# Kernel optimization log

Measured on AMD Instinct MI355X. Metric: run time of the kernel, lower is better.

The kernel has to match this reference:

```python
import jax, jax.numpy as jnp
import numpy as np

DIM = 1024
HEADS = 16
HEAD_DIM = DIM // HEADS
HIDDEN = 4096  # mlp_ratio * dim
SCALE = HEAD_DIM ** -0.5
LN_EPS = 1e-5


def softmax_one(x):
    # softmax with +1 in the denominator (after max subtraction), per source
    m = jnp.max(x, axis=-1, keepdims=True)
    e = jnp.exp(x - m)
    return e / (1.0 + jnp.sum(e, axis=-1, keepdims=True))


def layer_norm(x, g, b):
    mu = jnp.mean(x, axis=-1, keepdims=True)
    var = jnp.mean(jnp.square(x - mu), axis=-1, keepdims=True)
    return (x - mu) * jax.lax.rsqrt(var + LN_EPS) * g + b


def setup_inputs() -> dict:
    key = jax.random.key(0)
    ks = jax.random.split(key, 12)
    B, C, N = 2, DIM, 2048
    x = jax.random.normal(ks[0], (B, C, N), dtype=jnp.float32)
    mask = jax.random.randint(ks[1], (B, HEADS, N), 0, 2, dtype=jnp.int32)
    s = 0.02
    return {
        'x': x,
        'mask': mask,
        'qkv_w': jax.random.normal(ks[2], (3 * DIM, DIM), jnp.float32) * s,
        'qkv_b': jnp.zeros((3 * DIM,), jnp.float32),
        'proj_w': jax.random.normal(ks[3], (DIM, DIM), jnp.float32) * s,
        'proj_b': jnp.zeros((DIM,), jnp.float32),
        'fc1_w': jax.random.normal(ks[4], (HIDDEN, DIM), jnp.float32) * s,
        'fc1_b': jnp.zeros((HIDDEN,), jnp.float32),
        'ln_g': jnp.ones((HIDDEN,), jnp.float32),
        'ln_b': jnp.zeros((HIDDEN,), jnp.float32),
        'fc2_w': jax.random.normal(ks[5], (DIM, HIDDEN), jnp.float32) * s,
        'fc2_b': jnp.zeros((DIM,), jnp.float32),
    }


def reference(x, mask, qkv_w, qkv_b, proj_w, proj_b, fc1_w, fc1_b, ln_g, ln_b, fc2_w, fc2_b):
    B, C, N = x.shape
    xt = jnp.swapaxes(x, 1, 2)  # (B, N, C)

    # ----- attention -----
    qkv = xt @ qkv_w.T + qkv_b                      # (B, N, 3C)
    qkv = qkv.reshape(B, N, 3, HEADS, HEAD_DIM)
    qkv = jnp.transpose(qkv, (2, 0, 3, 1, 4))       # (3, B, H, N, Dh)
    q, k, v = qkv[0], qkv[1], qkv[2]
    scores = jnp.einsum('bhnd,bhmd->bhnm', q * SCALE, k)  # (B, H, N, N)
    scores = jnp.where(mask[:, :, :, None] == 0, -1e9, scores)
    attn = softmax_one(scores)
    out = jnp.einsum('bhnm,bhmd->bhnd', attn, v)    # (B, H, N, Dh)
    # faithful to source: permute(0,3,1,2).reshape(B,N,C) -> scrambled merge
    out = jnp.transpose(out, (0, 3, 1, 2)).reshape(B, N, C)
    out = out @ proj_w.T + proj_b

    # faithful residual: attn_out + ls1(attn_out) with ls1 = Identity
    h = out + out                                   # (B, N, C)

    # ----- MLP (timm Mlp: fc1 -> GELU -> LayerNorm -> fc2) -----
    m = h @ fc1_w.T + fc1_b
    m = jax.nn.gelu(m, approximate=False)
    m = layer_norm(m, ln_g, ln_b)
    m = m @ fc2_w.T + fc2_b
    y = h + m                                       # (B, N, C)

    return jnp.swapaxes(y, 1, 2)                    # (B, C, N)
```

## Files before the change

kernel.cpp:

```cpp
#include <hip/hip_runtime.h>
#include <math.h>

#define DIMC   1024
#define NTOK   2048
#define BATCH  2
#define HEADS  16
#define HDIM   64
#define HIDDEN 4096
#define MROWS  (BATCH*NTOK)
#define QSZ    ((size_t)BATCH*HEADS*NTOK*HDIM)
#define QSC    0.18033688f

typedef unsigned short ushort_t;
typedef __attribute__((ext_vector_type(8))) short short8;
typedef __attribute__((ext_vector_type(4))) float f32x4;
typedef __attribute__((ext_vector_type(4))) unsigned short us4;

__device__ __forceinline__ ushort_t f2b(float f) {
  union { float f; unsigned int u; } cv; cv.f = f;
  unsigned int u = cv.u;
  unsigned int r = (u + 0x7fffu + ((u >> 16) & 1u)) >> 16;
  return (ushort_t)r;
}

__device__ __forceinline__ float b2f(ushort_t b) {
  union { unsigned int u; float f; } cv; cv.u = ((unsigned int)b) << 16;
  return cv.f;
}

__device__ __forceinline__ float fexp2(float x) {
#if __has_builtin(__builtin_amdgcn_exp2f)
  return __builtin_amdgcn_exp2f(x);
#else
  return exp2f(x);
#endif
}

__device__ __forceinline__ void gl_lds16(const void* g, void* l) {
  __builtin_amdgcn_global_load_lds(
      (const __attribute__((address_space(1))) void*)g,
      (__attribute__((address_space(3))) void*)l, 16, 0, 0);
}

__global__ __launch_bounds__(256) void k_transpose(const float* __restrict__ x,
                                                   ushort_t* __restrict__ xt) {
  __shared__ float t[32][33];
  int b  = blockIdx.z;
  int c0 = blockIdx.y * 32, n0 = blockIdx.x * 32;
  int tx = threadIdx.x, ty = threadIdx.y;
#pragma unroll
  for (int l = 0; l < 4; l++)
    t[ty + l * 8][tx] = x[((size_t)(b * DIMC + c0 + ty + l * 8)) * NTOK + n0 + tx];
  __syncthreads();
#pragma unroll
  for (int l = 0; l < 4; l++)
    xt[((size_t)(b * NTOK + n0 + ty + l * 8)) * DIMC + c0 + tx] = f2b(t[tx][ty + l * 8]);
}

__global__ __launch_bounds__(256) void k_f2b4(const float* __restrict__ w0,
                                              const float* __restrict__ w1,
                                              const float* __restrict__ w2,
                                              const float* __restrict__ w3,
                                              ushort_t* __restrict__ o0,
                                              ushort_t* __restrict__ o1,
                                              ushort_t* __restrict__ o2,
                                              ushort_t* __restrict__ o3) {
  int bid = blockIdx.x;
  const float* in; ushort_t* out; int base;
  if (bid < 3072)      { in = w0; out = o0; base = bid; }
  else if (bid < 4096) { in = w1; out = o1; base = bid - 3072; }
  else if (bid < 8192) { in = w2; out = o2; base = bid - 4096; }
  else                 { in = w3; out = o3; base = bid - 8192; }
  int i = base * 256 + threadIdx.x;
  float4 v = ((const float4*)in)[i];
  us4 o; o.x = f2b(v.x); o.y = f2b(v.y); o.z = f2b(v.z); o.w = f2b(v.w);
  ((us4*)out)[i] = o;
}

template <int EPI, int NTX8, int KSTRIDE, int KLEN>
__global__ __launch_bounds__(256) void k_gemm_bf16(const ushort_t* __restrict__ A,
                                                   const ushort_t* __restrict__ W,
                                                   const float* __restrict__ bias,
                                                   void* __restrict__ outv) {
  __shared__ ushort_t As[2][128 * 32];
  __shared__ ushort_t Bs[2][128 * 32];
  const int tid = threadIdx.x;
  const int lane = tid & 63, wv = tid >> 6;
  const int bid = blockIdx.x, kz = blockIdx.y;
  const int xcd = bid & 7, t = bid >> 3;
  const int row0 = (t / NTX8) * 128;
  const int col0 = (xcd * NTX8 + (t % NTX8)) * 128;
  const int wrow0 = (wv >> 1) * 64, wcol0 = (wv & 1) * 64;
  const int lm = lane & 15, lq = lane >> 4;
  const int srow = wv * 32 + (lane >> 2);
  const int gch = (lane & 3) ^ ((lane >> 3) & 3);
  const int sw8 = (lq ^ ((lm >> 1) & 3)) * 8;

  const ushort_t* Ab = A + (size_t)(row0 + srow) * KSTRIDE + (size_t)kz * KLEN + gch * 8;
  const ushort_t* Wb = W + (size_t)(col0 + srow) * KSTRIDE + (size_t)kz * KLEN + gch * 8;
  const size_t rstep = (size_t)16 * KSTRIDE;

  f32x4 acc[4][4];
#pragma unroll
  for (int i = 0; i < 4; i++)
#pragma unroll
    for (int j = 0; j < 4; j++) acc[i][j] = (f32x4){0.f, 0.f, 0.f, 0.f};

#define STAGE(buf, k0) do {                                      \
    gl_lds16(Ab + (k0),         &As[buf][wv * 1024]);            \
    gl_lds16(Ab + rstep + (k0), &As[buf][wv * 1024 + 512]);      \
    gl_lds16(Wb + (k0),         &Bs[buf][wv * 1024]);            \
    gl_lds16(Wb + rstep + (k0), &Bs[buf][wv * 1024 + 512]);      \
  } while (0)

  auto compute = [&](int buf) {
    short8 af[4], bf[4];
#pragma unroll
    for (int mi = 0; mi < 4; mi++)
      af[mi] = *(const short8*)&As[buf][(wrow0 + mi * 16 + lm) * 32 + sw8];
#pragma unroll
    for (int ni = 0; ni < 4; ni++)
      bf[ni] = *(const short8*)&Bs[buf][(wcol0 + ni * 16 + lm) * 32 + sw8];
#pragma unroll
    for (int mi = 0; mi < 4; mi++)
#pragma unroll
      for (int ni = 0; ni < 4; ni++)
        acc[mi][ni] = __builtin_amdgcn_mfma_f32_16x16x32_bf16(af[mi], bf[ni], acc[mi][ni], 0, 0, 0);
  };

  constexpr int S = KLEN / 32;
  STAGE(0, 0);
#pragma unroll 1
  for (int kk = 0; kk < S; kk++) {
    __syncthreads();
    if (kk + 1 < S) STAGE((kk + 1) & 1, (kk + 1) * 32);
    compute(kk & 1);
  }
#undef STAGE

#pragma unroll
  for (int mi = 0; mi < 4; mi++) {
#pragma unroll
    for (int ni = 0; ni < 4; ni++) {
#pragma unroll
      for (int r = 0; r < 4; r++) {
        const int row = row0 + wrow0 + mi * 16 + lq * 4 + r;
        const int col = col0 + wcol0 + ni * 16 + lm;
        float v = acc[mi][ni][r];
        if (EPI != 4) v += bias[col];
        if (EPI == 0) {
          int which = col >> 10, rem = col & 1023, hh = rem >> 6, d = rem & 63;
          int bb = row >> 11, n = row & 2047;
          size_t bh = (size_t)(bb * HEADS + hh);
          ushort_t* o16 = (ushort_t*)outv;
          if (which == 0)
            o16[(bh * NTOK + n) * HDIM + d] = f2b(v * QSC);
          else if (which == 1)
            o16[QSZ + (bh * NTOK + n) * HDIM + d] = f2b(v);
          else
            o16[2 * QSZ + (bh * HDIM + d) * NTOK + n] = f2b(v);
        } else if (EPI == 2) {
          ((ushort_t*)outv)[(size_t)row * HIDDEN + col] = f2b(v);
        } else {
          ((float*)outv)[(size_t)kz * MROWS * DIMC + (size_t)row * DIMC + col] = v;
        }
      }
    }
  }
}

__global__ __launch_bounds__(256) void k_comb_proj(const float* __restrict__ p0,
                                                   const float* __restrict__ p1,
                                                   const float* __restrict__ bias,
                                                   ushort_t* __restrict__ hb) {
  int i = blockIdx.x * 256 + threadIdx.x;
  int colb = (i & 255) * 4;
  float4 a = ((const float4*)p0)[i];
  float4 b = ((const float4*)p1)[i];
  us4 o;
  o.x = f2b(2.f * (a.x + b.x + bias[colb + 0]));
  o.y = f2b(2.f * (a.y + b.y + bias[colb + 1]));
  o.z = f2b(2.f * (a.z + b.z + bias[colb + 2]));
  o.w = f2b(2.f * (a.w + b.w + bias[colb + 3]));
  ((us4*)hb)[i] = o;
}

__global__ __launch_bounds__(256) void k_comb_fc2(const float* __restrict__ p0,
                                                  const float* __restrict__ p1,
                                                  const ushort_t* __restrict__ hb,
                                                  const float* __restrict__ bias,
                                                  float* __restrict__ out) {
  __shared__ float t[32][33];
  int b  = blockIdx.z;
  int c0 = blockIdx.y * 32, n0 = blockIdx.x * 32;
  int tx = threadIdx.x, ty = threadIdx.y;
#pragma unroll
  for (int l = 0; l < 4; l++) {
    size_t idx = ((size_t)(b * NTOK + n0 + ty + l * 8)) * DIMC + c0 + tx;
    t[ty + l * 8][tx] = p0[idx] + p1[idx] + b2f(hb[idx]) + bias[c0 + tx];
  }
  __syncthreads();
#pragma unroll
  for (int l = 0; l < 4; l++)
    out[((size_t)(b * DIMC + c0 + ty + l * 8)) * NTOK + n0 + tx] = t[tx][ty + l * 8];
}

__global__ __launch_bounds__(256) void k_attn_mfma(const ushort_t* __restrict__ qkv,
                                                   const int* __restrict__ mask,
                                                   ushort_t* __restrict__ scram) {
  __shared__ ushort_t Kl[2][64 * 64];
  __shared__ ushort_t Vl[2][64 * 64];
  __shared__ ushort_t Pl[4 * 16 * 72];
  const int tid = threadIdx.x;
  const int lane = tid & 63, w = tid >> 6;
  const int lm = lane & 15, quad = lane >> 4;
  const int bh = blockIdx.y, b = bh >> 4, h = bh & 15;
  const int q0 = blockIdx.x * 64 + w * 16;
  const ushort_t* qg  = qkv + (size_t)bh * NTOK * HDIM;
  const ushort_t* kg  = qkv + QSZ + (size_t)bh * NTOK * HDIM;
  const ushort_t* vTg = qkv + 2 * QSZ + (size_t)bh * HDIM * NTOK;
  ushort_t* Pw = &Pl[w * 16 * 72];

  const short8 ones = {0x3F80, 0x3F80, 0x3F80, 0x3F80, 0x3F80, 0x3F80, 0x3F80, 0x3F80};

  short8 qf[2];
#pragma unroll
  for (int hf = 0; hf < 2; hf++)
    qf[hf] = *(const short8*)&qg[(size_t)(q0 + lm) * HDIM + hf * 32 + quad * 8];

  bool mk[4];
#pragma unroll
  for (int r = 0; r < 4; r++)
    mk[r] = mask[(size_t)bh * NTOK + q0 + quad * 4 + r] != 0;

  f32x4 O[4], La;
  La = (f32x4){0.f, 0.f, 0.f, 0.f};
#pragma unroll
  for (int r = 0; r < 4; r++) O[r] = (f32x4){0.f, 0.f, 0.f, 0.f};

  const int s0 = tid, s1 = tid + 256;
  const int r0 = s0 >> 3, g0 = (s0 & 7) ^ (r0 & 7);
  const int r1 = s1 >> 3, g1 = (s1 & 7) ^ (r1 & 7);

  gl_lds16(kg + (size_t)r0 * HDIM + g0 * 8, &Kl[0][s0 * 8]);
  gl_lds16(kg + (size_t)r1 * HDIM + g1 * 8, &Kl[0][s1 * 8]);
  gl_lds16(vTg + (size_t)r0 * NTOK + g0 * 8, &Vl[0][s0 * 8]);
  gl_lds16(vTg + (size_t)r1 * NTOK + g1 * 8, &Vl[0][s1 * 8]);

  for (int kt = 0; kt < NTOK; kt += 64) {
    const int cur = (kt >> 6) & 1, nxt = cur ^ 1;
    __syncthreads();
    if (kt + 64 < NTOK) {
      gl_lds16(kg + (size_t)(kt + 64 + r0) * HDIM + g0 * 8, &Kl[nxt][s0 * 8]);
      gl_lds16(kg + (size_t)(kt + 64 + r1) * HDIM + g1 * 8, &Kl[nxt][s1 * 8]);
      gl_lds16(vTg + (size_t)r0 * NTOK + kt + 64 + g0 * 8, &Vl[nxt][s0 * 8]);
      gl_lds16(vTg + (size_t)r1 * NTOK + kt + 64 + g1 * 8, &Vl[nxt][s1 * 8]);
    }

    short8 kf[4][2];
#pragma unroll
    for (int ksub = 0; ksub < 4; ksub++)
#pragma unroll
      for (int hf = 0; hf < 2; hf++)
        kf[ksub][hf] = *(const short8*)&Kl[cur][(ksub * 16 + lm) * 64 + ((4 * hf + quad) ^ (lm & 7)) * 8];

    short8 vf[4][2];
#pragma unroll
    for (int dsub = 0; dsub < 4; dsub++)
#pragma unroll
      for (int hf = 0; hf < 2; hf++)
        vf[dsub][hf] = *(const short8*)&Vl[cur][(dsub * 16 + lm) * 64 + ((4 * hf + quad) ^ (lm & 7)) * 8];

    f32x4 S[4];
#pragma unroll
    for (int ksub = 0; ksub < 4; ksub++) {
      S[ksub] = (f32x4){0.f, 0.f, 0.f, 0.f};
      S[ksub] = __builtin_amdgcn_mfma_f32_16x16x32_bf16(qf[0], kf[ksub][0], S[ksub], 0, 0, 0);
      S[ksub] = __builtin_amdgcn_mfma_f32_16x16x32_bf16(qf[1], kf[ksub][1], S[ksub], 0, 0, 0);
    }
#pragma unroll
    for (int r = 0; r < 4; r++) {
      const int prow = quad * 4 + r;
#pragma unroll
      for (int ksub = 0; ksub < 4; ksub++) {
        float p = mk[r] ? fexp2(S[ksub][r]) : 1.0f;
        Pw[prow * 72 + ksub * 16 + lm] = (ushort_t)(__float_as_uint(p) >> 16);
      }
    }
    __builtin_amdgcn_s_waitcnt(0xC07F);

    short8 pf[2];
#pragma unroll
    for (int hf = 0; hf < 2; hf++)
      pf[hf] = *(const short8*)&Pw[lm * 72 + hf * 32 + quad * 8];
#pragma unroll
    for (int dsub = 0; dsub < 4; dsub++) {
      O[dsub] = __builtin_amdgcn_mfma_f32_16x16x32_bf16(pf[0], vf[dsub][0], O[dsub], 0, 0, 0);
      O[dsub] = __builtin_amdgcn_mfma_f32_16x16x32_bf16(pf[1], vf[dsub][1], O[dsub], 0, 0, 0);
    }
    La = __builtin_amdgcn_mfma_f32_16x16x32_bf16(pf[0], ones, La, 0, 0, 0);
    La = __builtin_amdgcn_mfma_f32_16x16x32_bf16(pf[1], ones, La, 0, 0, 0);
  }

#pragma unroll
  for (int r = 0; r < 4; r++) {
    int n = q0 + quad * 4 + r;
    float inv = 1.f / (1.f + La[r]);
    int n1 = n >> 10, nn0 = n & 1023;
#pragma unroll
    for (int dsub = 0; dsub < 4; dsub++) {
      int d = dsub * 16 + lm;
      int np = d * 32 + h * 2 + n1;
      scram[((size_t)(b * NTOK + np)) * DIMC + nn0] = f2b(O[dsub][r] * inv);
    }
  }
}

__global__ __launch_bounds__(256) void k_ln(ushort_t* __restrict__ mid,
                                            const float* __restrict__ g,
                                            const float* __restrict__ bta) {
  const int row = blockIdx.x;
  ushort_t* p = mid + (size_t)row * HIDDEN;
  const int tid = threadIdx.x;
  float lv[16];
  float s = 0.f, s2 = 0.f;
#pragma unroll
  for (int i = 0; i < 4; i++) {
    us4 u = *(const us4*)&p[tid * 4 + i * 1024];
#pragma unroll
    for (int j = 0; j < 4; j++) {
      float xx = b2f((j == 0) ? u.x : (j == 1) ? u.y : (j == 2) ? u.z : u.w);
      xx = 0.5f * xx * (1.f + erff(xx * 0.70710678118654752f));
      lv[i * 4 + j] = xx;
      s += xx;
      s2 += xx * xx;
    }
  }
#pragma unroll
  for (int off = 32; off > 0; off >>= 1) {
    s += __shfl_down(s, off);
    s2 += __shfl_down(s2, off);
  }
  __shared__ float rs[4], rs2[4];
  if ((tid & 63) == 0) { rs[tid >> 6] = s; rs2[tid >> 6] = s2; }
  __syncthreads();
  float ts = rs[0] + rs[1] + rs[2] + rs[3];
  float ts2 = rs2[0] + rs2[1] + rs2[2] + rs2[3];
  float mu = ts * (1.f / HIDDEN);
  float var = ts2 * (1.f / HIDDEN) - mu * mu;
  float rstd = rsqrtf(var + 1e-5f);
#pragma unroll
  for (int i = 0; i < 4; i++) {
    us4 o;
#pragma unroll
    for (int j = 0; j < 4; j++) {
      int f = tid * 4 + i * 1024 + j;
      float y = (lv[i * 4 + j] - mu) * rstd * g[f] + bta[f];
      ushort_t ob = f2b(y);
      if (j == 0) o.x = ob; else if (j == 1) o.y = ob; else if (j == 2) o.z = ob; else o.w = ob;
    }
    *(us4*)&p[tid * 4 + i * 1024] = o;
  }
}

extern "C" void kernel_launch(void* const* d_in, const int* in_sizes, int n_in,
                              void* d_out, int out_size, void* d_ws, size_t ws_size,
                              hipStream_t stream) {
  const float* x      = (const float*)d_in[0];
  const int*   mask   = (const int*)d_in[1];
  const float* qkv_w  = (const float*)d_in[2];
  const float* qkv_b  = (const float*)d_in[3];
  const float* proj_w = (const float*)d_in[4];
  const float* proj_b = (const float*)d_in[5];
  const float* fc1_w  = (const float*)d_in[6];
  const float* fc1_b  = (const float*)d_in[7];
  const float* ln_g   = (const float*)d_in[8];
  const float* ln_b   = (const float*)d_in[9];
  const float* fc2_w  = (const float*)d_in[10];
  const float* fc2_b  = (const float*)d_in[11];

  char* w = (char*)d_ws;
  ushort_t* qkv16  = (ushort_t*)w;           w += 3 * QSZ * 2;
  ushort_t* xtb    = (ushort_t*)w;           w += (size_t)MROWS * DIMC * 2;
  ushort_t* scramb = (ushort_t*)w;           w += (size_t)MROWS * DIMC * 2;
  ushort_t* hb     = (ushort_t*)w;           w += (size_t)MROWS * DIMC * 2;
  ushort_t* mid    = (ushort_t*)w;           w += (size_t)MROWS * HIDDEN * 2;
  ushort_t* wqkvb  = (ushort_t*)w;           w += (size_t)3 * DIMC * DIMC * 2;
  ushort_t* wprojb = (ushort_t*)w;           w += (size_t)DIMC * DIMC * 2;
  ushort_t* wfc1b  = (ushort_t*)w;           w += (size_t)HIDDEN * DIMC * 2;
  ushort_t* wfc2b  = (ushort_t*)w;           w += (size_t)DIMC * HIDDEN * 2;
  float*    pbuf   = (float*)w;              w += (size_t)2 * MROWS * DIMC * 4;
  float*    pbuf1  = pbuf + (size_t)MROWS * DIMC;

  k_transpose<<<dim3(NTOK / 32, DIMC / 32, BATCH), dim3(32, 8), 0, stream>>>(x, xtb);
  k_f2b4<<<dim3(12288), 256, 0, stream>>>(qkv_w, proj_w, fc1_w, fc2_w,
                                          wqkvb, wprojb, wfc1b, wfc2b);

  k_gemm_bf16<0, 3, DIMC, DIMC><<<dim3(24 * 32), 256, 0, stream>>>(
      xtb, wqkvb, qkv_b, qkv16);
  k_attn_mfma<<<dim3(NTOK / 64, BATCH * HEADS), 256, 0, stream>>>(
      qkv16, mask, scramb);
  k_gemm_bf16<4, 1, DIMC, 512><<<dim3(8 * 32, 2), 256, 0, stream>>>(
      scramb, wprojb, nullptr, pbuf);
  k_comb_proj<<<dim3(4096), 256, 0, stream>>>(pbuf, pbuf1, proj_b, hb);
  k_gemm_bf16<2, 4, DIMC, DIMC><<<dim3(32 * 32), 256, 0, stream>>>(
      hb, wfc1b, fc1_b, mid);
  k_ln<<<dim3(MROWS), 256, 0, stream>>>(mid, ln_g, ln_b);
  k_gemm_bf16<4, 1, HIDDEN, 2048><<<dim3(8 * 32, 2), 256, 0, stream>>>(
      mid, wfc2b, nullptr, pbuf);
  k_comb_fc2<<<dim3(NTOK / 32, DIMC / 32, BATCH), dim3(32, 8), 0, stream>>>(
      pbuf, pbuf1, hb, fc2_b, (float*)d_out);
}
```

Baseline: 405.7 us.

## Switch attention kernel to 32x32x16 MFMA with 32 queries per wave

Rewrites the attention inner loop to use 32x32x16 bf16 MFMA instructions, with each wave now handling 32 query rows (128 per block) instead of 16. S is computed transposed (K as the A operand) so that exp'd probabilities can be packed into pairs and written to a swizzled per-wave LDS tile with 64-bit stores. The goal is to halve K/V tile reloads per query and cut LDS traffic per FLOP. The cost is fewer blocks (half the grid), higher register use from the 16-wide accumulators, and a more intricate layout mapping that must match the scrambled output indexing.

Measured after the change: 387.6 us. -4.5%, faster.

```diff
diff --git a/kernel.cpp b/kernel.cpp
--- a/kernel.cpp
+++ b/kernel.cpp
@@ -14,7 +14,9 @@
 typedef unsigned short ushort_t;
 typedef __attribute__((ext_vector_type(8))) short short8;
 typedef __attribute__((ext_vector_type(4))) float f32x4;
+typedef __attribute__((ext_vector_type(16))) float f32x16;
 typedef __attribute__((ext_vector_type(4))) unsigned short us4;
+typedef __attribute__((ext_vector_type(2))) unsigned int u32x2;
 
 __device__ __forceinline__ ushort_t f2b(float f) {
   union { float f; unsigned int u; } cv; cv.f = f;
@@ -210,33 +212,30 @@
                                                    ushort_t* __restrict__ scram) {
   __shared__ ushort_t Kl[2][64 * 64];
   __shared__ ushort_t Vl[2][64 * 64];
-  __shared__ ushort_t Pl[4 * 16 * 72];
+  __shared__ ushort_t Pl[4][32 * 64];
   const int tid = threadIdx.x;
   const int lane = tid & 63, w = tid >> 6;
-  const int lm = lane & 15, quad = lane >> 4;
+  const int l31 = lane & 31, hi = lane >> 5;
+  const int sw = l31 & 7;
   const int bh = blockIdx.y, b = bh >> 4, h = bh & 15;
-  const int q0 = blockIdx.x * 64 + w * 16;
+  const int q0 = blockIdx.x * 128 + w * 32;
   const ushort_t* qg  = qkv + (size_t)bh * NTOK * HDIM;
   const ushort_t* kg  = qkv + QSZ + (size_t)bh * NTOK * HDIM;
   const ushort_t* vTg = qkv + 2 * QSZ + (size_t)bh * HDIM * NTOK;
-  ushort_t* Pw = &Pl[w * 16 * 72];
+  ushort_t* Pw = &Pl[w][0];
 
   const short8 ones = {0x3F80, 0x3F80, 0x3F80, 0x3F80, 0x3F80, 0x3F80, 0x3F80, 0x3F80};
 
-  short8 qf[2];
-#pragma unroll
-  for (int hf = 0; hf < 2; hf++)
-    qf[hf] = *(const short8*)&qg[(size_t)(q0 + lm) * HDIM + hf * 32 + quad * 8];
-
-  bool mk[4];
-#pragma unroll
-  for (int r = 0; r < 4; r++)
-    mk[r] = mask[(size_t)bh * NTOK + q0 + quad * 4 + r] != 0;
-
-  f32x4 O[4], La;
-  La = (f32x4){0.f, 0.f, 0.f, 0.f};
-#pragma unroll
-  for (int r = 0; r < 4; r++) O[r] = (f32x4){0.f, 0.f, 0.f, 0.f};
+  short8 qf[4];
+#pragma unroll
+  for (int c = 0; c < 4; c++)
+    qf[c] = *(const short8*)&qg[(size_t)(q0 + l31) * HDIM + c * 16 + hi * 8];
+
+  const bool mkq = mask[(size_t)bh * NTOK + q0 + l31] != 0;
+
+  f32x16 O0, O1, La;
+#pragma unroll
+  for (int i = 0; i < 16; i++) { O0[i] = 0.f; O1[i] = 0.f; La[i] = 0.f; }
 
   const int s0 = tid, s1 = tid + 256;
   const int r0 = s0 >> 3, g0 = (s0 & 7) ^ (r0 & 7);
@@ -257,61 +256,66 @@
       gl_lds16(vTg + (size_t)r1 * NTOK + kt + 64 + g1 * 8, &Vl[nxt][s1 * 8]);
     }
 
-    short8 kf[4][2];
-#pragma unroll
-    for (int ksub = 0; ksub < 4; ksub++)
-#pragma unroll
-      for (int hf = 0; hf < 2; hf++)
-        kf[ksub][hf] = *(const short8*)&Kl[cur][(ksub * 16 + lm) * 64 + ((4 * hf + quad) ^ (lm & 7)) * 8];
-
-    short8 vf[4][2];
-#pragma unroll
-    for (int dsub = 0; dsub < 4; dsub++)
-#pragma unroll
-      for (int hf = 0; hf < 2; hf++)
-        vf[dsub][hf] = *(const short8*)&Vl[cur][(dsub * 16 + lm) * 64 + ((4 * hf + quad) ^ (lm & 7)) * 8];
-
-    f32x4 S[4];
-#pragma unroll
-    for (int ksub = 0; ksub < 4; ksub++) {
-      S[ksub] = (f32x4){0.f, 0.f, 0.f, 0.f};
-      S[ksub] = __builtin_amdgcn_mfma_f32_16x16x32_bf16(qf[0], kf[ksub][0], S[ksub], 0, 0, 0);
-      S[ksub] = __builtin_amdgcn_mfma_f32_16x16x32_bf16(qf[1], kf[ksub][1], S[ksub], 0, 0, 0);
-    }
-#pragma unroll
-    for (int r = 0; r < 4; r++) {
-      const int prow = quad * 4 + r;
-#pragma unroll
-      for (int ksub = 0; ksub < 4; ksub++) {
-        float p = mk[r] ? fexp2(S[ksub][r]) : 1.0f;
-        Pw[prow * 72 + ksub * 16 + lm] = (ushort_t)(__float_as_uint(p) >> 16);
+    f32x16 S[2];
+#pragma unroll
+    for (int i = 0; i < 16; i++) { S[0][i] = 0.f; S[1][i] = 0.f; }
+#pragma unroll
+    for (int c = 0; c < 4; c++) {
+      short8 kf0 = *(const short8*)&Kl[cur][(l31) * 64 + ((2 * c + hi) ^ sw) * 8];
+      short8 kf1 = *(const short8*)&Kl[cur][(32 + l31) * 64 + ((2 * c + hi) ^ sw) * 8];
+      S[0] = __builtin_amdgcn_mfma_f32_32x32x16_bf16(kf0, qf[c], S[0], 0, 0, 0);
+      S[1] = __builtin_amdgcn_mfma_f32_32x32x16_bf16(kf1, qf[c], S[1], 0, 0, 0);
+    }
+
+    short8 vf[2][4];
+#pragma unroll
+    for (int dh = 0; dh < 2; dh++)
+#pragma unroll
+      for (int cc = 0; cc < 4; cc++)
+        vf[dh][cc] = *(const short8*)&Vl[cur][(dh * 32 + l31) * 64 + ((2 * cc + hi) ^ sw) * 8];
+
+    unsigned int pd[2][8];
+#pragma unroll
+    for (int H = 0; H < 2; H++)
+#pragma unroll
+      for (int tt = 0; tt < 8; tt++) {
+        float p0 = mkq ? fexp2(S[H][2 * tt])     : 1.0f;
+        float p1 = mkq ? fexp2(S[H][2 * tt + 1]) : 1.0f;
+        pd[H][tt] = (__float_as_uint(p1) & 0xFFFF0000u) | (__float_as_uint(p0) >> 16);
       }
-    }
+
+#pragma unroll
+    for (int H = 0; H < 2; H++)
+#pragma unroll
+      for (int a = 0; a < 4; a++)
+        *(u32x2*)&Pw[l31 * 64 + (((4 * H + a) ^ sw) * 8) + hi * 4] =
+            (u32x2){pd[H][2 * a], pd[H][2 * a + 1]};
     __builtin_amdgcn_s_waitcnt(0xC07F);
 
-    short8 pf[2];
-#pragma unroll
-    for (int hf = 0; hf < 2; hf++)
-      pf[hf] = *(const short8*)&Pw[lm * 72 + hf * 32 + quad * 8];
-#pragma unroll
-    for (int dsub = 0; dsub < 4; dsub++) {
-      O[dsub] = __builtin_amdgcn_mfma_f32_16x16x32_bf16(pf[0], vf[dsub][0], O[dsub], 0, 0, 0);
-      O[dsub] = __builtin_amdgcn_mfma_f32_16x16x32_bf16(pf[1], vf[dsub][1], O[dsub], 0, 0, 0);
-    }
-    La = __builtin_amdgcn_mfma_f32_16x16x32_bf16(pf[0], ones, La, 0, 0, 0);
-    La = __builtin_amdgcn_mfma_f32_16x16x32_bf16(pf[1], ones, La, 0, 0, 0);
-  }
-
-#pragma unroll
-  for (int r = 0; r < 4; r++) {
-    int n = q0 + quad * 4 + r;
-    float inv = 1.f / (1.f + La[r]);
+#pragma unroll
+    for (int cc = 0; cc < 4; cc++) {
+      short8 pf = *(const short8*)&Pw[l31 * 64 + ((2 * cc + hi) ^ sw) * 8];
+      O0 = __builtin_amdgcn_mfma_f32_32x32x16_bf16(pf, vf[0][cc], O0, 0, 0, 0);
+      O1 = __builtin_amdgcn_mfma_f32_32x32x16_bf16(pf, vf[1][cc], O1, 0, 0, 0);
+      La = __builtin_amdgcn_mfma_f32_32x32x16_bf16(pf, ones, La, 0, 0, 0);
+    }
+  }
+
+#pragma unroll
+  for (int reg = 0; reg < 16; reg++) {
+    int qp = (reg & 3) + 8 * (reg >> 2) + 4 * hi;
+    int n = q0 + qp;
+    float inv = 1.f / (1.f + La[reg]);
     int n1 = n >> 10, nn0 = n & 1023;
-#pragma unroll
-    for (int dsub = 0; dsub < 4; dsub++) {
-      int d = dsub * 16 + lm;
+    {
+      int d = l31;
       int np = d * 32 + h * 2 + n1;
-      scram[((size_t)(b * NTOK + np)) * DIMC + nn0] = f2b(O[dsub][r] * inv);
+      scram[((size_t)(b * NTOK + np)) * DIMC + nn0] = f2b(O0[reg] * inv);
+    }
+    {
+      int d = 32 + l31;
+      int np = d * 32 + h * 2 + n1;
+      scram[((size_t)(b * NTOK + np)) * DIMC + nn0] = f2b(O1[reg] * inv);
     }
   }
 }
@@ -398,7 +402,7 @@
 
   k_gemm_bf16<0, 3, DIMC, DIMC><<<dim3(24 * 32), 256, 0, stream>>>(
       xtb, wqkvb, qkv_b, qkv16);
-  k_attn_mfma<<<dim3(NTOK / 64, BATCH * HEADS), 256, 0, stream>>>(
+  k_attn_mfma<<<dim3(NTOK / 128, BATCH * HEADS), 256, 0, stream>>>(
       qkv16, mask, scramb);
   k_gemm_bf16<4, 1, DIMC, 512><<<dim3(8 * 32, 2), 256, 0, stream>>>(
       scramb, wprojb, nullptr, pbuf);
```
